# Kernel tuning notes

Measured on AMD Instinct MI355X. Metric: run time of the kernel, lower is better.

The kernel has to match this reference:

```python
import jax, jax.numpy as jnp
import numpy as np

NUM_HEADS = 16
NUM_BUCKETS = 32
MAX_DISTANCE = 128


def _relative_position_bucket(relative_position, num_buckets=NUM_BUCKETS, max_distance=MAX_DISTANCE):
    # bidirectional=True (encoder self-attention)
    nb = num_buckets // 2  # 16
    buckets = (relative_position > 0).astype(jnp.int32) * nb
    rp = jnp.abs(relative_position)
    max_exact = nb // 2  # 8
    is_small = rp < max_exact
    # log-spaced bins for large distances; clamp arg of log to >=1 to avoid log(0)
    rp_f = jnp.maximum(rp, 1).astype(jnp.float32)
    large = max_exact + (
        jnp.log(rp_f / max_exact) / np.log(max_distance / max_exact) * (nb - max_exact)
    ).astype(jnp.int32)
    large = jnp.minimum(large, nb - 1)
    return buckets + jnp.where(is_small, rp, large)


def setup_inputs() -> dict:
    key = jax.random.key(0)
    ks = jax.random.split(key, 6)
    B, L, D = 2, 2048, 1024
    scale = 0.02  # keep activations in a sane range
    return {
        "hidden_states": jax.random.normal(ks[0], (B, L, D), dtype=jnp.float32),
        "Wq": jax.random.normal(ks[1], (D, D), dtype=jnp.float32) * scale,
        "Wk": jax.random.normal(ks[2], (D, D), dtype=jnp.float32) * scale,
        "Wv": jax.random.normal(ks[3], (D, D), dtype=jnp.float32) * scale,
        "Wo": jax.random.normal(ks[4], (D, D), dtype=jnp.float32) * scale,
        "bias_table": jax.random.normal(ks[5], (NUM_BUCKETS, NUM_HEADS), dtype=jnp.float32),
    }


def reference(hidden_states, Wq, Wk, Wv, Wo, bias_table):
    B, L, D = hidden_states.shape
    H = NUM_HEADS
    hd = D // H

    # projections (nn.Linear: y = x @ W.T), split heads -> [B, H, L, hd]
    def proj(x, W):
        return (x @ W.T).reshape(B, L, H, hd).transpose(0, 2, 1, 3)

    q = proj(hidden_states, Wq)
    k = proj(hidden_states, Wk)
    v = proj(hidden_states, Wv)

    # T5 relative position bias: [1, H, L, L]
    ctx = jnp.arange(L)[:, None]
    mem = jnp.arange(L)[None, :]
    buckets = _relative_position_bucket(mem - ctx)  # [L, L]
    position_bias = bias_table[buckets].transpose(2, 0, 1)[None]  # [1, H, L, L]

    # NOTE: T5-style attention has NO 1/sqrt(hd) scaling
    scores = jnp.einsum("bhqd,bhkd->bhqk", q, k) + position_bias
    attn = jax.nn.softmax(scores.astype(jnp.float32), axis=-1).astype(scores.dtype)
    out = jnp.einsum("bhqk,bhkd->bhqd", attn, v)
    out = out.transpose(0, 2, 1, 3).reshape(B, L, D)
    out = out @ Wo.T
    return out, position_bias
```

## Files before the change

kernel.cpp:

```cpp
#include <hip/hip_runtime.h>
#include <cstdint>
#include <cmath>

typedef unsigned short ushort_t;
typedef __bf16 bf16x8 __attribute__((ext_vector_type(8)));
typedef float f32x4 __attribute__((ext_vector_type(4)));
typedef ushort_t us4 __attribute__((ext_vector_type(4)));
typedef ushort_t us8 __attribute__((ext_vector_type(8)));

#define MFMA16(a, b, c) __builtin_amdgcn_mfma_f32_16x16x32_bf16(a, b, c, 0, 0, 0)
#define LOG2E 1.4426950408889634f

__device__ __forceinline__ ushort_t f2bf(float f) {
    union { __bf16 h; ushort_t u; } cv;
    cv.h = (__bf16)f;
    return cv.u;
}

__device__ __forceinline__ void glds16(const ushort_t* g, ushort_t* s) {
    __builtin_amdgcn_global_load_lds(
        (const __attribute__((address_space(1))) void*)(g),
        (__attribute__((address_space(3))) void*)(s), 16, 0, 0);
}

__global__ void cast_all_k(const float* __restrict__ x, const float* __restrict__ wq,
                           const float* __restrict__ wk, const float* __restrict__ wv,
                           const float* __restrict__ wo, ushort_t* __restrict__ xb,
                           ushort_t* __restrict__ wb, unsigned char* __restrict__ lut) {
    int id = blockIdx.x, t = threadIdx.x;
    if (id == 8192) {
        for (int idx = t; idx < 4095; idx += 256) {
            int rel = idx - 2047;
            int bb = (rel > 0) ? 16 : 0;
            int rp = (rel < 0) ? -rel : rel;
            int add;
            if (rp < 8) {
                add = rp;
            } else {
                float lg = (float)::log((double)rp * 0.125);
                double tt = ((double)lg) / 2.772588722239781 * 8.0;
                int large = 8 + (int)tt;
                add = (large < 15) ? large : 15;
            }
            lut[idx] = (unsigned char)(bb + add);
        }
        return;
    }
    const float* src;
    ushort_t* dst;
    int idx;
    float scale = 1.0f;
    if (id < 4096) {
        src = x; dst = xb; idx = id * 256 + t;
    } else {
        int r = (id - 4096) >> 10;
        idx = ((id - 4096) & 1023) * 256 + t;
        src = (r == 0) ? wq : (r == 1) ? wk : (r == 2) ? wv : wo;
        dst = wb + (size_t)r * 1048576;
        if (r == 0) scale = LOG2E;
    }
    float4 v = ((const float4*)src)[idx];
    us4 o;
    o.x = f2bf(v.x * scale); o.y = f2bf(v.y * scale);
    o.z = f2bf(v.z * scale); o.w = f2bf(v.w * scale);
    ((us4*)dst)[idx] = o;
}

template <int MODE>
__global__ __launch_bounds__(256) void gemm_bt_k(const ushort_t* __restrict__ A,
                                                 const ushort_t* __restrict__ B0,
                                                 void* __restrict__ C0,
                                                 int M, int N, int K, long sB, long sC) {
    __shared__ ushort_t As[128 * 64];
    __shared__ ushort_t Bs[128 * 64];
    const int tid = threadIdx.x;
    const int l = tid & 63, w = tid >> 6;
    const int quad = l >> 4, lc = l & 15;
    const int wm = w >> 1, wn = w & 1;
    const int m0 = blockIdx.y * 128, n0 = blockIdx.x * 128;
    const ushort_t* B = B0 + (long)blockIdx.z * sB;

    f32x4 acc[4][4] = {};
    const int rA = l >> 3;
    const int cA = ((l & 7) ^ rA) * 8;

    for (int k0 = 0; k0 < K; k0 += 64) {
#pragma unroll
        for (int t = 0; t < 4; ++t) {
            int row = w * 32 + t * 8;
            glds16(A + (size_t)(m0 + row + rA) * K + k0 + cA, &As[row * 64]);
            glds16(B + (size_t)(n0 + row + rA) * K + k0 + cA, &Bs[row * 64]);
        }
        __syncthreads();
#pragma unroll
        for (int ko = 0; ko < 2; ++ko) {
            const int ch = (((ko * 4 + quad) ^ (lc & 7))) * 8;
            bf16x8 af[4], bfr[4];
#pragma unroll
            for (int mt = 0; mt < 4; ++mt)
                af[mt] = *(const bf16x8*)&As[(wm * 64 + mt * 16 + lc) * 64 + ch];
#pragma unroll
            for (int nt = 0; nt < 4; ++nt)
                bfr[nt] = *(const bf16x8*)&Bs[(wn * 64 + nt * 16 + lc) * 64 + ch];
#pragma unroll
            for (int mt = 0; mt < 4; ++mt)
#pragma unroll
                for (int nt = 0; nt < 4; ++nt)
                    acc[mt][nt] = MFMA16(af[mt], bfr[nt], acc[mt][nt]);
        }
        __syncthreads();
    }
#pragma unroll
    for (int mt = 0; mt < 4; ++mt) {
#pragma unroll
        for (int nt = 0; nt < 4; ++nt) {
            int col = n0 + wn * 64 + nt * 16 + lc;
#pragma unroll
            for (int r = 0; r < 4; ++r) {
                int row = m0 + wm * 64 + mt * 16 + quad * 4 + r;
                if constexpr (MODE == 1) {
                    ((float*)C0)[(size_t)row * N + col] = acc[mt][nt][r];
                } else if constexpr (MODE == 0) {
                    (((ushort_t*)C0) + (long)blockIdx.z * sC)[(size_t)row * N + col] = f2bf(acc[mt][nt][r]);
                } else {
                    ((ushort_t*)C0)[(size_t)(col >> 11) * 2097152 + (size_t)row * 2048 + (col & 2047)] =
                        f2bf(acc[mt][nt][r]);
                }
            }
        }
    }
}

__global__ __launch_bounds__(256, 2) void attn_k(const ushort_t* __restrict__ Qg,
                                                 const ushort_t* __restrict__ Kg,
                                                 const ushort_t* __restrict__ VTg,
                                                 ushort_t* __restrict__ Ctx,
                                                 const unsigned char* __restrict__ lut,
                                                 const float* __restrict__ table,
                                                 float* __restrict__ bias_out) {
    __shared__ ushort_t Kbuf[2][128 * 64];
    __shared__ ushort_t Pws[4 * 32 * 40];
    __shared__ float diag[2][256];

    const int tid = threadIdx.x, l = tid & 63, w = tid >> 6;
    const int quad = l >> 4, lc = l & 15;
    const int id = blockIdx.x;
    const int bh = id & 31, b = bh >> 4, h = bh & 15;
    const int q0 = (id >> 5) * 128;
    const size_t tokbase = (size_t)b * 2048;

    const int rK = l >> 3;
    const int cK = ((l & 7) ^ rK) * 8;

#pragma unroll
    for (int t = 0; t < 4; ++t) {
        int row0 = w * 32 + t * 8;
        glds16(Qg + (tokbase + q0 + row0 + rK) * 1024 + h * 64 + cK, &Kbuf[1][row0 * 64]);
        glds16(Kg + (tokbase + row0 + rK) * 1024 + h * 64 + cK, &Kbuf[0][row0 * 64]);
    }
    if (tid < 255) diag[0][tid] = table[(int)lut[tid + 1920 - q0] * 16 + h];
    __syncthreads();

    bf16x8 qf[2][2];
#pragma unroll
    for (int nt = 0; nt < 2; ++nt)
#pragma unroll
        for (int ko = 0; ko < 2; ++ko) {
            int row = w * 32 + nt * 16 + lc;
            int ch = ((ko * 4 + quad) ^ (lc & 7)) * 8;
            qf[nt][ko] = *(const bf16x8*)&Kbuf[1][row * 64 + ch];
        }
    __syncthreads();

    float mstate[2] = {-1e30f, -1e30f};
    float lstate[2] = {0.f, 0.f};
    f32x4 acco[4][2] = {};
    ushort_t* Pw = &Pws[w * 1280];
    const int cb0 = quad * 4 - (w * 32 + lc) + 127;
    const int cxor = lc & 3;
    const ushort_t* VTbase = VTg + (size_t)(b * 1024 + h * 64) * 2048;

    const int bjf = (tid & 15) * 4 + b * 64;
    const int big = tid >> 4;

    for (int kt = 0; kt < 16; ++kt) {
        const int j0 = kt * 128;
        const int cur = kt & 1, nxt = cur ^ 1;
        const ushort_t* Kc = Kbuf[cur];
        const float* dc = diag[cur];

        if (kt < 15) {
            const int jn = j0 + 128;
#pragma unroll
            for (int t = 0; t < 4; ++t) {
                int row0 = w * 32 + t * 8;
                glds16(Kg + (tokbase + jn + row0 + rK) * 1024 + h * 64 + cK, &Kbuf[nxt][row0 * 64]);
            }
            if (tid < 255) diag[nxt][tid] = table[(int)lut[jn - q0 + tid + 1920] * 16 + h];
        }

        bf16x8 vf[4][4];
#pragma unroll
        for (int kk = 0; kk < 4; ++kk)
#pragma unroll
            for (int dt = 0; dt < 4; ++dt)
                vf[kk][dt] = *(const bf16x8*)(VTbase + (size_t)(dt * 16 + lc) * 2048 +
                                              j0 + kk * 32 + quad * 8);

        {
            float* outp = bias_out + ((size_t)h * 2048 + q0) * 2048 + j0;
#pragma unroll
            for (int rr = 0; rr < 8; ++rr) {
                int il = big + 16 * rr;
                int d0 = bjf - il + 127;
                f32x4 v;
                v[0] = dc[d0]; v[1] = dc[d0 + 1]; v[2] = dc[d0 + 2]; v[3] = dc[d0 + 3];
                __builtin_nontemporal_store(v, (f32x4*)(outp + (size_t)il * 2048 + bjf));
            }
        }

        f32x4 accs[8][2] = {};
#pragma unroll
        for (int ko = 0; ko < 2; ++ko) {
            const int ch = ((ko * 4 + quad) ^ (lc & 7)) * 8;
#pragma unroll
            for (int mt = 0; mt < 8; ++mt) {
                bf16x8 kf = *(const bf16x8*)&Kc[(mt * 16 + lc) * 64 + ch];
                accs[mt][0] = MFMA16(kf, qf[0][ko], accs[mt][0]);
                accs[mt][1] = MFMA16(kf, qf[1][ko], accs[mt][1]);
            }
        }

        float dprev[4], dcur[4];
#pragma unroll
        for (int r = 0; r < 4; ++r) dprev[r] = dc[cb0 - 16 + r];
#pragma unroll
        for (int mt = 0; mt < 8; ++mt) {
#pragma unroll
            for (int r = 0; r < 4; ++r) dcur[r] = dc[cb0 + mt * 16 + r];
#pragma unroll
            for (int r = 0; r < 4; ++r) {
                accs[mt][0][r] = fmaf(dcur[r], LOG2E, accs[mt][0][r]);
                accs[mt][1][r] = fmaf(dprev[r], LOG2E, accs[mt][1][r]);
            }
#pragma unroll
            for (int r = 0; r < 4; ++r) dprev[r] = dcur[r];
        }

#pragma unroll
        for (int nt = 0; nt < 2; ++nt) {
            float mx = accs[0][nt][0];
#pragma unroll
            for (int mt = 0; mt < 8; ++mt)
#pragma unroll
                for (int r = 0; r < 4; ++r) mx = fmaxf(mx, accs[mt][nt][r]);
            mx = fmaxf(mx, __shfl_xor(mx, 16, 64));
            mx = fmaxf(mx, __shfl_xor(mx, 32, 64));
            float mo = mstate[nt], mn = fmaxf(mo, mx);
            float alpha = __builtin_amdgcn_exp2f(mo - mn);
            mstate[nt] = mn;
            float rs = 0.f;
#pragma unroll
            for (int mt = 0; mt < 8; ++mt)
#pragma unroll
                for (int r = 0; r < 4; ++r) {
                    float p = __builtin_amdgcn_exp2f(accs[mt][nt][r] - mn);
                    accs[mt][nt][r] = p;
                    rs += p;
                }
            rs += __shfl_xor(rs, 16, 64);
            rs += __shfl_xor(rs, 32, 64);
            lstate[nt] = lstate[nt] * alpha + rs;
#pragma unroll
            for (int dt = 0; dt < 4; ++dt) acco[dt][nt] *= alpha;
        }

#pragma unroll
        for (int kk = 0; kk < 4; ++kk) {
#pragma unroll
            for (int half = 0; half < 2; ++half) {
                int mt = kk * 2 + half;
                int c = half * 2 + (quad >> 1);
                int coff = ((c ^ cxor) * 8 + (quad & 1) * 4);
#pragma unroll
                for (int nt = 0; nt < 2; ++nt) {
                    us4 o;
#pragma unroll
                    for (int r = 0; r < 4; ++r) o[r] = f2bf(accs[mt][nt][r]);
                    *(us4*)&Pw[(nt * 16 + lc) * 40 + coff] = o;
                }
            }
            bf16x8 pf[2];
#pragma unroll
            for (int nt = 0; nt < 2; ++nt)
                pf[nt] = *(const bf16x8*)&Pw[(nt * 16 + lc) * 40 + (quad ^ cxor) * 8];
#pragma unroll
            for (int dt = 0; dt < 4; ++dt)
#pragma unroll
                for (int nt = 0; nt < 2; ++nt)
                    acco[dt][nt] = MFMA16(vf[kk][dt], pf[nt], acco[dt][nt]);
        }
        if (kt < 15) __syncthreads();
    }

#pragma unroll
    for (int nt = 0; nt < 2; ++nt) {
        float inv = 1.0f / lstate[nt];
        size_t row = tokbase + q0 + w * 32 + nt * 16 + lc;
#pragma unroll
        for (int dt = 0; dt < 4; ++dt) {
            us4 o;
#pragma unroll
            for (int r = 0; r < 4; ++r) o[r] = f2bf(acco[dt][nt][r] * inv);
            *(us4*)&Ctx[row * 1024 + h * 64 + dt * 16 + quad * 4] = o;
        }
    }
}

extern "C" void kernel_launch(void* const* d_in, const int* in_sizes, int n_in,
                              void* d_out, int out_size, void* d_ws, size_t ws_size,
                              hipStream_t stream) {
    const float* hidden = (const float*)d_in[0];
    const float* Wq = (const float*)d_in[1];
    const float* Wk = (const float*)d_in[2];
    const float* Wv = (const float*)d_in[3];
    const float* Wo = (const float*)d_in[4];
    const float* table = (const float*)d_in[5];

    char* ws = (char*)d_ws;
    ushort_t* Xb  = (ushort_t*)(ws);
    ushort_t* Wb  = (ushort_t*)(ws + 8388608);
    ushort_t* Qg  = (ushort_t*)(ws + 16777216);
    ushort_t* Kgp = (ushort_t*)(ws + 25165824);
    ushort_t* VTg = (ushort_t*)(ws + 33554432);
    ushort_t* Ctx = (ushort_t*)(ws + 41943040);
    unsigned char* lutp = (unsigned char*)(ws + 50331648);

    float* out0 = (float*)d_out;
    float* out1 = out0 + 4194304;

    cast_all_k<<<8193, 256, 0, stream>>>(hidden, Wq, Wk, Wv, Wo, Xb, Wb, lutp);

    gemm_bt_k<0><<<dim3(8, 32, 2), 256, 0, stream>>>(Xb, Wb, (void*)Qg,
                                                     4096, 1024, 1024, 1048576, 4194304);
    gemm_bt_k<2><<<dim3(32, 8, 1), 256, 0, stream>>>(Wb + 2097152, Xb, (void*)VTg,
                                                     1024, 4096, 1024, 0, 0);
    attn_k<<<dim3(512), 256, 0, stream>>>(Qg, Kgp, VTg, Ctx, lutp, table, out1);
    gemm_bt_k<1><<<dim3(8, 32, 1), 256, 0, stream>>>(Ctx, Wb + 3145728, (void*)out0,
                                                     4096, 1024, 1024, 0, 0);
}
```

Measured before the change: 426.8 us.

## Drop shared-memory K staging and block barriers; load K/Q directly per wave

Removes the shared-memory double buffer for K and Q and the per-tile block-wide barriers. Each wave now reads its Q fragments and all K fragments directly from global memory and keeps its own private copy of the diagonal bias buffer. V fragments are also double-buffered in registers, one 32-column chunk ahead, instead of all being loaded up front. This removes barrier stalls and lowers register and LDS pressure, at the cost of each K tile being fetched four times per block from L2/global with unswizzled, less coalesced loads.

```diff
diff --git a/kernel.cpp b/kernel.cpp
--- a/kernel.cpp
+++ b/kernel.cpp
@@ -138,9 +138,8 @@
                                                  const unsigned char* __restrict__ lut,
                                                  const float* __restrict__ table,
                                                  float* __restrict__ bias_out) {
-    __shared__ ushort_t Kbuf[2][128 * 64];
     __shared__ ushort_t Pws[4 * 32 * 40];
-    __shared__ float diag[2][256];
+    __shared__ float diagw[4][2][256];
 
     const int tid = threadIdx.x, l = tid & 63, w = tid >> 6;
     const int quad = l >> 4, lc = l & 15;
@@ -149,28 +148,31 @@
     const int q0 = (id >> 5) * 128;
     const size_t tokbase = (size_t)b * 2048;
 
-    const int rK = l >> 3;
-    const int cK = ((l & 7) ^ rK) * 8;
-
-#pragma unroll
-    for (int t = 0; t < 4; ++t) {
-        int row0 = w * 32 + t * 8;
-        glds16(Qg + (tokbase + q0 + row0 + rK) * 1024 + h * 64 + cK, &Kbuf[1][row0 * 64]);
-        glds16(Kg + (tokbase + row0 + rK) * 1024 + h * 64 + cK, &Kbuf[0][row0 * 64]);
-    }
-    if (tid < 255) diag[0][tid] = table[(int)lut[tid + 1920 - q0] * 16 + h];
-    __syncthreads();
+    const ushort_t* Qrow = Qg + (tokbase + q0) * 1024 + h * 64;
+    const ushort_t* Krow = Kg + tokbase * 1024 + h * 64;
+    const ushort_t* VTbase = VTg + (size_t)(b * 1024 + h * 64) * 2048;
 
     bf16x8 qf[2][2];
 #pragma unroll
     for (int nt = 0; nt < 2; ++nt)
 #pragma unroll
-        for (int ko = 0; ko < 2; ++ko) {
-            int row = w * 32 + nt * 16 + lc;
-            int ch = ((ko * 4 + quad) ^ (lc & 7)) * 8;
-            qf[nt][ko] = *(const bf16x8*)&Kbuf[1][row * 64 + ch];
-        }
-    __syncthreads();
+        for (int ko = 0; ko < 2; ++ko)
+            qf[nt][ko] = *(const bf16x8*)(Qrow + (size_t)(w * 32 + nt * 16 + lc) * 1024 +
+                                          ko * 32 + quad * 8);
+
+    float* dgbuf0 = &diagw[w][0][0];
+    float* dgbuf1 = &diagw[w][1][0];
+    {
+        int base = 1920 - q0;
+        f32x4 v;
+#pragma unroll
+        for (int e = 0; e < 4; ++e) {
+            int li = base + l * 4 + e;
+            li = (li < 4094) ? li : 4094;
+            v[e] = table[(int)lut[li] * 16 + h];
+        }
+        *(f32x4*)&dgbuf0[l * 4] = v;
+    }
 
     float mstate[2] = {-1e30f, -1e30f};
     float lstate[2] = {0.f, 0.f};
@@ -178,34 +180,43 @@
     ushort_t* Pw = &Pws[w * 1280];
     const int cb0 = quad * 4 - (w * 32 + lc) + 127;
     const int cxor = lc & 3;
-    const ushort_t* VTbase = VTg + (size_t)(b * 1024 + h * 64) * 2048;
 
     const int bjf = (tid & 15) * 4 + b * 64;
     const int big = tid >> 4;
 
     for (int kt = 0; kt < 16; ++kt) {
         const int j0 = kt * 128;
-        const int cur = kt & 1, nxt = cur ^ 1;
-        const ushort_t* Kc = Kbuf[cur];
-        const float* dc = diag[cur];
+        float* dc = (kt & 1) ? dgbuf1 : dgbuf0;
+        float* dn = (kt & 1) ? dgbuf0 : dgbuf1;
 
         if (kt < 15) {
-            const int jn = j0 + 128;
-#pragma unroll
-            for (int t = 0; t < 4; ++t) {
-                int row0 = w * 32 + t * 8;
-                glds16(Kg + (tokbase + jn + row0 + rK) * 1024 + h * 64 + cK, &Kbuf[nxt][row0 * 64]);
-            }
-            if (tid < 255) diag[nxt][tid] = table[(int)lut[jn - q0 + tid + 1920] * 16 + h];
-        }
-
-        bf16x8 vf[4][4];
-#pragma unroll
-        for (int kk = 0; kk < 4; ++kk)
-#pragma unroll
-            for (int dt = 0; dt < 4; ++dt)
-                vf[kk][dt] = *(const bf16x8*)(VTbase + (size_t)(dt * 16 + lc) * 2048 +
-                                              j0 + kk * 32 + quad * 8);
+            int base = j0 + 128 - q0 + 1920;
+            f32x4 v;
+#pragma unroll
+            for (int e = 0; e < 4; ++e) {
+                int li = base + l * 4 + e;
+                li = (li < 4094) ? li : 4094;
+                v[e] = table[(int)lut[li] * 16 + h];
+            }
+            *(f32x4*)&dn[l * 4] = v;
+        }
+
+        f32x4 accs[8][2] = {};
+#pragma unroll
+        for (int ko = 0; ko < 2; ++ko) {
+#pragma unroll
+            for (int mt = 0; mt < 8; ++mt) {
+                bf16x8 kf = *(const bf16x8*)(Krow + (size_t)(j0 + mt * 16 + lc) * 1024 +
+                                             ko * 32 + quad * 8);
+                accs[mt][0] = MFMA16(kf, qf[0][ko], accs[mt][0]);
+                accs[mt][1] = MFMA16(kf, qf[1][ko], accs[mt][1]);
+            }
+        }
+
+        bf16x8 vfp[2][4];
+#pragma unroll
+        for (int dt = 0; dt < 4; ++dt)
+            vfp[0][dt] = *(const bf16x8*)(VTbase + (size_t)(dt * 16 + lc) * 2048 + j0 + quad * 8);
 
         {
             float* outp = bias_out + ((size_t)h * 2048 + q0) * 2048 + j0;
@@ -216,18 +227,6 @@
                 f32x4 v;
                 v[0] = dc[d0]; v[1] = dc[d0 + 1]; v[2] = dc[d0 + 2]; v[3] = dc[d0 + 3];
                 __builtin_nontemporal_store(v, (f32x4*)(outp + (size_t)il * 2048 + bjf));
-            }
-        }
-
-        f32x4 accs[8][2] = {};
-#pragma unroll
-        for (int ko = 0; ko < 2; ++ko) {
-            const int ch = ((ko * 4 + quad) ^ (lc & 7)) * 8;
-#pragma unroll
-            for (int mt = 0; mt < 8; ++mt) {
-                bf16x8 kf = *(const bf16x8*)&Kc[(mt * 16 + lc) * 64 + ch];
-                accs[mt][0] = MFMA16(kf, qf[0][ko], accs[mt][0]);
-                accs[mt][1] = MFMA16(kf, qf[1][ko], accs[mt][1]);
             }
         }
 
@@ -277,6 +276,13 @@
 
 #pragma unroll
         for (int kk = 0; kk < 4; ++kk) {
+            if (kk < 3) {
+#pragma unroll
+                for (int dt = 0; dt < 4; ++dt)
+                    vfp[(kk + 1) & 1][dt] =
+                        *(const bf16x8*)(VTbase + (size_t)(dt * 16 + lc) * 2048 +
+                                         j0 + (kk + 1) * 32 + quad * 8);
+            }
 #pragma unroll
             for (int half = 0; half < 2; ++half) {
                 int mt = kk * 2 + half;
@@ -298,9 +304,8 @@
             for (int dt = 0; dt < 4; ++dt)
 #pragma unroll
                 for (int nt = 0; nt < 2; ++nt)
-                    acco[dt][nt] = MFMA16(vf[kk][dt], pf[nt], acco[dt][nt]);
-        }
-        if (kt < 15) __syncthreads();
+                    acco[dt][nt] = MFMA16(vfp[kk & 1][dt], pf[nt], acco[dt][nt]);
+        }
     }
 
 #pragma unroll
```

Result: slower. 469.7 us (+10.0%).
